# Performance work log

Hardware: AMD Instinct MI355X
Metric: run time of the kernel (lower is better)

Reference implementation:

```python
import jax, jax.numpy as jnp
import numpy as np

N_EMBD = 2048
N_HEAD = 16
HEAD_DIM = N_EMBD // N_HEAD
LORA_R = 8
LORA_ALPHA = 1.0
LORA_SCALING = LORA_ALPHA / LORA_R


def setup_inputs() -> dict:
    key = jax.random.key(0)
    ks = jax.random.split(key, 10)
    B, T = 4, 2048
    init = LORA_ALPHA / LORA_R
    return {
        "x": jax.random.normal(ks[0], (B, T, N_EMBD), dtype=jnp.float32),
        "W_attn": jax.random.normal(ks[1], (N_EMBD, 3 * N_EMBD), dtype=jnp.float32) * 0.02,
        "b_attn": jnp.zeros((3 * N_EMBD,), dtype=jnp.float32),
        "lora_A_q": jax.random.normal(ks[2], (N_EMBD, LORA_R), dtype=jnp.float32) * init,
        "lora_B_q": jax.random.normal(ks[3], (LORA_R, N_EMBD), dtype=jnp.float32) * init,
        "lora_A_k": jax.random.normal(ks[4], (N_EMBD, LORA_R), dtype=jnp.float32) * init,
        "lora_B_k": jax.random.normal(ks[5], (LORA_R, N_EMBD), dtype=jnp.float32) * init,
        "W_proj": jax.random.normal(ks[6], (N_EMBD, N_EMBD), dtype=jnp.float32) * 0.02,
        "b_proj": jnp.zeros((N_EMBD,), dtype=jnp.float32),
    }


def _rotate_half(x):
    # torch: x1 = x[..., ::2]; x2 = x[..., 1::2]; cat((-x2, x1), -1)
    x1 = x[..., ::2]
    x2 = x[..., 1::2]
    return jnp.concatenate([-x2, x1], axis=-1)


def _rope_cos_sin(T, dtype):
    inv_freq = 1.0 / (10000.0 ** (jnp.arange(0, HEAD_DIM, 2, dtype=jnp.float32) / HEAD_DIM))
    t = jnp.arange(T, dtype=jnp.float32)
    freqs = jnp.einsum("i,j->ij", t, inv_freq)            # [T, D/2]
    emb = jnp.concatenate([freqs, freqs], axis=-1)          # [T, D]
    return jnp.cos(emb).astype(dtype), jnp.sin(emb).astype(dtype)


def reference(x, W_attn, b_attn, lora_A_q, lora_B_q, lora_A_k, lora_B_k, W_proj, b_proj):
    B, T, C = x.shape
    qkv = x @ W_attn + b_attn                                # [B,T,3C]
    q, k, v = jnp.split(qkv, 3, axis=2)
    # LoRA additions on q, k (applied to attn outputs, per module)
    q = q + (q @ lora_A_q) @ lora_B_q * LORA_SCALING
    k = k + (k @ lora_A_k) @ lora_B_k * LORA_SCALING

    def to_heads(z):
        return z.reshape(B, T, N_HEAD, HEAD_DIM).transpose(0, 2, 1, 3)  # [B,H,T,D]

    q, k, v = to_heads(q), to_heads(k), to_heads(v)
    cos, sin = _rope_cos_sin(T, x.dtype)                     # [T,D] each
    q = q * cos + _rotate_half(q) * sin
    k = k * cos + _rotate_half(k) * sin

    scale = 1.0 / jnp.sqrt(jnp.asarray(HEAD_DIM, dtype=x.dtype))
    scores = jnp.einsum("bhqd,bhkd->bhqk", q, k) * scale     # [B,H,T,T]
    causal = jnp.tril(jnp.ones((T, T), dtype=bool))
    scores = jnp.where(causal, scores, jnp.finfo(x.dtype).min)
    attn = jax.nn.softmax(scores, axis=-1)
    y = jnp.einsum("bhqk,bhkd->bhqd", attn, v)               # [B,H,T,D]
    y = y.transpose(0, 2, 1, 3).reshape(B, T, C)
    return y @ W_proj + b_proj
```

## Files before the change

### kernel.cpp

```cpp
#include <hip/hip_runtime.h>
#include <stdint.h>


typedef __attribute__((ext_vector_type(8))) short short8;
typedef __attribute__((ext_vector_type(4))) short short4v;
typedef __attribute__((ext_vector_type(4))) float floatx4;

__device__ __forceinline__ float bf2f(short h) {
  union { unsigned int u; float f; } v;
  v.u = ((unsigned int)(unsigned short)h) << 16;
  return v.f;
}
__device__ __forceinline__ short f2bf(float f) {
  unsigned int u = __float_as_uint(f);
  unsigned int r = (u + 0x7FFFu + ((u >> 16) & 1u)) >> 16;
  return (short)r;
}

__device__ __forceinline__ void gload_lds16(const short* g, short* l) {
  __builtin_amdgcn_global_load_lds(
      (const __attribute__((address_space(1))) unsigned int*)g,
      (__attribute__((address_space(3))) unsigned int*)l, 16, 0, 0);
}

__device__ __forceinline__ void store_out(float* p, float v) { *p = v; }
__device__ __forceinline__ void store_out(short* p, float v) { *p = f2bf(v); }

__device__ __forceinline__ int xcd_swz(int orig, int nwg) {
  int q = nwg >> 3;
  return (orig & 7) * q + (orig >> 3);
}

#define SWZ(off, row) ((off) ^ (((row) & 7) << 3))

__global__ void k_f2b(const float* __restrict__ in, short* __restrict__ out, int n8) {
  int i = blockIdx.x * 256 + threadIdx.x;
  if (i >= n8) return;
  const float4* p = (const float4*)in + (size_t)i * 2;
  float4 a = p[0], b = p[1];
  short8 v;
  v[0] = f2bf(a.x); v[1] = f2bf(a.y); v[2] = f2bf(a.z); v[3] = f2bf(a.w);
  v[4] = f2bf(b.x); v[5] = f2bf(b.y); v[6] = f2bf(b.z); v[7] = f2bf(b.w);
  *(short8*)(out + (size_t)i * 8) = v;
}

__global__ void k_wT(const float* __restrict__ W, short* __restrict__ WT, int K, int N) {
  __shared__ float tile[32][33];
  int n0 = blockIdx.x * 32, k0 = blockIdx.y * 32;
  int tx = threadIdx.x, ty = threadIdx.y;
  #pragma unroll
  for (int i = 0; i < 4; i++)
    tile[ty + i * 8][tx] = W[(size_t)(k0 + ty + i * 8) * N + n0 + tx];
  __syncthreads();
  #pragma unroll
  for (int i = 0; i < 4; i++)
    WT[(size_t)(n0 + ty + i * 8) * K + k0 + tx] = f2bf(tile[tx][ty + i * 8]);
}

__global__ void k_ropetab(float* __restrict__ ct, float* __restrict__ st) {
  int t = blockIdx.x, j = threadIdx.x;
  float invf = powf(10000.0f, -(float)(2 * j) / 128.0f);
  float ang = (float)t * invf;
  ct[t * 64 + j] = cosf(ang);
  st[t * 64 + j] = sinf(ang);
}


#define GBAR __builtin_amdgcn_s_barrier();

#define RDA(QR) \
    _Pragma("unroll") for (int m_ = 0; m_ < 4; m_++) \
    _Pragma("unroll") for (int kk_ = 0; kk_ < 2; kk_++) { \
      int sA_ = ((QR) * 2 + wm) * 8192 + (m_ * 16 + c16) * 128 + kk_ * 64 + g * 16; \
      afr[m_][kk_] = *(const short8*)(Ab + ((sA_ ^ swzk) >> 1)); \
    }

#define RDB(QC, DST) \
    _Pragma("unroll") for (int n_ = 0; n_ < 2; n_++) \
    _Pragma("unroll") for (int kk_ = 0; kk_ < 2; kk_++) { \
      int sB_ = ((QC) * 4 + wn) * 4096 + (n_ * 16 + c16) * 128 + kk_ * 64 + g * 16; \
      DST[n_][kk_] = *(const short8*)(Bb + ((sB_ ^ swzk) >> 1)); \
    }

#define MM(QR, QC, BF) \
    __builtin_amdgcn_s_barrier(); \
    __builtin_amdgcn_s_setprio(1); \
    _Pragma("unroll") for (int kk_ = 0; kk_ < 2; kk_++) \
    _Pragma("unroll") for (int m_ = 0; m_ < 4; m_++) \
    _Pragma("unroll") for (int n_ = 0; n_ < 2; n_++) \
      acc[(QR) * 4 + m_][(QC) * 2 + n_] = __builtin_amdgcn_mfma_f32_16x16x32_bf16( \
          afr[m_][kk_], BF[n_][kk_], acc[(QR) * 4 + m_][(QC) * 2 + n_], 0, 0, 0); \
    __builtin_amdgcn_s_setprio(0);

template <typename OutT>
__global__ __launch_bounds__(512, 2) void k_gemm8(
    const short* __restrict__ A, const short* __restrict__ BT,
    const float* __restrict__ bias, OutT* __restrict__ C,
    int M, int N, int K)
{
  __shared__ __attribute__((aligned(16))) short lds[65536];
  const int tid = threadIdx.x;
  const int w = tid >> 6, l = tid & 63;
  const int g = l >> 4, c16 = l & 15;
  const int wm = w >> 2, wn = w & 3;
  const int swzk = (c16 & 7) << 4;

  const int nwg = gridDim.x * gridDim.y;
  const int wg = xcd_swz(blockIdx.y * gridDim.x + blockIdx.x, nwg);
  const int bm = wg % gridDim.x, bn = wg / gridDim.x;

  const short* Ablk = A + (size_t)bm * 256 * K;
  const short* Bblk = BT + (size_t)bn * 256 * K;

  floatx4 acc[8][4];
  #pragma unroll
  for (int i = 0; i < 8; i++)
    #pragma unroll
    for (int j = 0; j < 4; j++)
      acc[i][j] = (floatx4){0.f, 0.f, 0.f, 0.f};

  const int NT = K >> 6;
  const int L = NT >> 1;

  auto stageA = [&](int b, int h, int t) {
    short* dst = lds + b * 32768;
    int k0 = t * 64;
    #pragma unroll
    for (int j = 0; j < 2; j++) {
      int P = h * 2 + j;
      int sL = P * 8192 + tid * 16;
      int q = sL ^ (((sL >> 7) & 7) << 4);
      int row = (((((P & 1) << 1) | (P >> 1))) << 6) + ((sL >> 7) & 63);
      gload_lds16(Ablk + (size_t)row * K + k0 + ((q & 127) >> 1), dst + (sL >> 1));
    }
  };
  auto stageB = [&](int b, int h, int t) {
    short* dst = lds + b * 32768 + 16384;
    int k0 = t * 64;
    #pragma unroll
    for (int j = 0; j < 2; j++) {
      int sL = (h * 4 + 2 * j) * 4096 + tid * 16;
      int pos = sL >> 12;
      int q = sL ^ (((sL >> 7) & 7) << 4);
      int row = (((pos & 3) * 2 + (pos >> 2)) << 5) + ((sL >> 7) & 31);
      gload_lds16(Bblk + (size_t)row * K + k0 + ((q & 127) >> 1), dst + (sL >> 1));
    }
  };

  stageA(0, 0, 0); stageB(0, 0, 0); stageA(0, 1, 0); stageB(0, 1, 0);
  stageA(1, 0, 1); stageB(1, 0, 1); stageA(1, 1, 1); stageB(1, 1, 1);
  asm volatile("s_waitcnt vmcnt(8)" ::: "memory");
  __builtin_amdgcn_s_barrier();

  #pragma unroll 1
  for (int i = 0; i < L; i++) {
    const int t2 = 2 * i + 2, t3 = 2 * i + 3;
    short8 afr[4][2], bfr0[2][2], bfr1[2][2];

    {
      const short* Ab = lds;
      const short* Bb = lds + 16384;
      RDA(0) RDB(0, bfr0) if (i > 0) stageA(1, 1, 2 * i + 1);
      MM(0, 0, bfr0) GBAR
      RDB(1, bfr1) if (t2 < NT) stageA(0, 0, t2);
      MM(0, 1, bfr1) GBAR
      RDA(1) if (t2 < NT) stageB(0, 0, t2);
      MM(1, 0, bfr0) GBAR
      if (t2 < NT) stageB(0, 1, t2);
      MM(1, 1, bfr1)
      if (t2 < NT) { asm volatile("s_waitcnt vmcnt(6)" ::: "memory"); }
      else         { asm volatile("s_waitcnt vmcnt(0)" ::: "memory"); }
      GBAR
    }
    {
      const short* Ab = lds + 32768;
      const short* Bb = lds + 49152;
      RDA(0) RDB(0, bfr0) if (t2 < NT) stageA(0, 1, t2);
      MM(0, 0, bfr0) GBAR
      RDB(1, bfr1) if (t3 < NT) stageA(1, 0, t3);
      MM(0, 1, bfr1) GBAR
      RDA(1) if (t3 < NT) stageB(1, 0, t3);
      MM(1, 0, bfr0) GBAR
      if (t3 < NT) stageB(1, 1, t3);
      MM(1, 1, bfr1)
      if (t3 < NT) { asm volatile("s_waitcnt vmcnt(6)" ::: "memory"); }
      else         { asm volatile("s_waitcnt vmcnt(0)" ::: "memory"); }
      GBAR
    }
  }

  #pragma unroll
  for (int qr = 0; qr < 2; qr++)
    #pragma unroll
    for (int qc = 0; qc < 2; qc++)
      #pragma unroll
      for (int m = 0; m < 4; m++)
        #pragma unroll
        for (int n = 0; n < 2; n++) {
          int col = bn * 256 + wn * 64 + qc * 32 + n * 16 + c16;
          float bv = bias[col];
          #pragma unroll
          for (int r = 0; r < 4; r++) {
            size_t row = (size_t)bm * 256 + wm * 128 + qr * 64 + m * 16 + g * 4 + r;
            store_out(C + row * (size_t)N + col, acc[qr * 4 + m][qc * 2 + n][r] + bv);
          }
        }
}

__global__ __launch_bounds__(256, 2) void k_lorarope(
    short* __restrict__ qkv, const float* __restrict__ Aq, const float* __restrict__ Ak,
    const float* __restrict__ Bq, const float* __restrict__ Bk,
    const float* __restrict__ ct, const float* __restrict__ st)
{
  __shared__ float Bs[8 * 2048];
  __shared__ short Ls[2048];
  __shared__ float red[4][8];
  const int u = threadIdx.x;
  const int which = blockIdx.y;
  const float* Am = which ? Ak : Aq;
  const float* Bm = which ? Bk : Bq;
  const float qs = which ? 1.0f : 0.08838834764831845f;

  #pragma unroll
  for (int i = 0; i < 16; i++) {
    int idx = (i * 256 + u) * 4;
    *(float4*)(Bs + idx) = *(const float4*)(Bm + idx);
  }
  float Areg[8][8];
  #pragma unroll
  for (int e = 0; e < 8; e++) {
    float4 a0 = *(const float4*)(Am + (size_t)(u * 8 + e) * 8);
    float4 a1 = *(const float4*)(Am + (size_t)(u * 8 + e) * 8 + 4);
    Areg[e][0] = a0.x; Areg[e][1] = a0.y; Areg[e][2] = a0.z; Areg[e][3] = a0.w;
    Areg[e][4] = a1.x; Areg[e][5] = a1.y; Areg[e][6] = a1.z; Areg[e][7] = a1.w;
  }
  __syncthreads();

  const int wv = u >> 6, l = u & 63;
  const int h = u >> 4, j0 = (u & 15) * 4;
  const int base = h * 128;
  const int t0 = blockIdx.x * 32;

  for (int tt = 0; tt < 32; tt++) {
    const int tok = t0 + tt;
    const int trow = tok & 2047;
    short* row = qkv + (size_t)tok * 6144 + which * 2048;

    __syncthreads();

    short8 q8 = *(const short8*)(row + u * 8);
    *(short8*)(Ls + u * 8) = q8;
    float part[8];
    #pragma unroll
    for (int r = 0; r < 8; r++) part[r] = 0.f;
    #pragma unroll
    for (int e = 0; e < 8; e++) {
      float qv = bf2f(q8[e]);
      #pragma unroll
      for (int r = 0; r < 8; r++) part[r] += qv * Areg[e][r];
    }
    #pragma unroll
    for (int r = 0; r < 8; r++)
      for (int off = 32; off > 0; off >>= 1)
        part[r] += __shfl_xor(part[r], off);
    if (l == 0) {
      #pragma unroll
      for (int r = 0; r < 8; r++) red[wv][r] = part[r];
    }
    __syncthreads();

    float Tr[8];
    #pragma unroll
    for (int r = 0; r < 8; r++)
      Tr[r] = (red[0][r] + red[1][r] + red[2][r] + red[3][r]) * 0.125f;

    float4 cv = *(const float4*)(ct + trow * 64 + j0);
    float4 sv = *(const float4*)(st + trow * 64 + j0);
    short4v qa4 = *(const short4v*)(Ls + base + j0);
    short4v qb4 = *(const short4v*)(Ls + base + 64 + j0);
    short8 qeo = *(const short8*)(Ls + base + 2 * j0);

    float o1[4], o2[4];
    #pragma unroll
    for (int j = 0; j < 4; j++) {
      float da = 0.f, db = 0.f, de = 0.f, dd = 0.f;
      #pragma unroll
      for (int r = 0; r < 8; r++) {
        const float* Br = Bs + r * 2048 + base;
        da += Tr[r] * Br[j0 + j];
        db += Tr[r] * Br[64 + j0 + j];
        de += Tr[r] * Br[2 * (j0 + j)];
        dd += Tr[r] * Br[2 * (j0 + j) + 1];
      }
      float qa = bf2f(qa4[j]) + da;
      float qb = bf2f(qb4[j]) + db;
      float qe = bf2f(qeo[2 * j]) + de;
      float qo = bf2f(qeo[2 * j + 1]) + dd;
      float c = ((const float*)&cv)[j], s = ((const float*)&sv)[j];
      o1[j] = (qa * c - qo * s) * qs;
      o2[j] = (qb * c + qe * s) * qs;
    }
    short4v w1, w2;
    #pragma unroll
    for (int j = 0; j < 4; j++) { w1[j] = f2bf(o1[j]); w2[j] = f2bf(o2[j]); }
    *(short4v*)(row + base + j0) = w1;
    *(short4v*)(row + base + 64 + j0) = w2;
  }
}

__global__ void k_vt(const short* __restrict__ qkv, short* __restrict__ vT) {
  __shared__ short tile[32][33];
  int bh = blockIdx.z, b = bh >> 4, h = bh & 15;
  int t0 = blockIdx.x * 32, d0 = blockIdx.y * 32;
  int tx = threadIdx.x, ty = threadIdx.y;
  #pragma unroll
  for (int i = 0; i < 4; i++) {
    int tt = t0 + ty + i * 8;
    tile[ty + i * 8][tx] = qkv[(size_t)(b * 2048 + tt) * 6144 + 4096 + h * 128 + d0 + tx];
  }
  __syncthreads();
  #pragma unroll
  for (int i = 0; i < 4; i++) {
    int d = d0 + ty + i * 8;
    vT[((size_t)bh * 128 + d) * 2048 + t0 + tx] = tile[tx][ty + i * 8];
  }
}

__global__ __launch_bounds__(256, 2) void k_attn(
    const short* __restrict__ qkv, const short* __restrict__ vT, short* __restrict__ y)
{
  __shared__ __attribute__((aligned(16))) short Ks[64 * 128];
  __shared__ __attribute__((aligned(16))) short Vs[128 * 64];
  __shared__ __attribute__((aligned(16))) short Ps[4 * 32 * 64];
  const int bh = blockIdx.x, b = bh >> 4, h = bh & 15;
  const int qt = 15 - (int)blockIdx.y;
  const int t = threadIdx.x, w = t >> 6, l = t & 63, g = l >> 4, c16 = l & 15;

  const int skr = t >> 2, sc0 = (t & 3) * 32;
  const int svd = t >> 1, sv0 = (t & 1) * 32;
  const short* kbase = qkv + (size_t)(b * 2048) * 6144 + 2048 + h * 128;
  const short* vbase = vT + (size_t)bh * 128 * 2048;
  short* Pw = Ps + w * (32 * 64);

  short8 onesv;
  #pragma unroll
  for (int e = 0; e < 8; e++) onesv[e] = (short)0x3F80;

  short8 qf[2][4];
  #pragma unroll
  for (int m = 0; m < 2; m++) {
    size_t goff = (size_t)(b * 2048 + qt * 128 + w * 32 + m * 16 + c16) * 6144 + h * 128;
    #pragma unroll
    for (int kf = 0; kf < 4; kf++)
      qf[m][kf] = *(const short8*)(qkv + goff + kf * 32 + 8 * g);
  }

  floatx4 o[2][8], ls[2];
  float mrow[2][4];
  #pragma unroll
  for (int m = 0; m < 2; m++) {
    #pragma unroll
    for (int nf = 0; nf < 8; nf++) o[m][nf] = (floatx4){0.f, 0.f, 0.f, 0.f};
    ls[m] = (floatx4){0.f, 0.f, 0.f, 0.f};
    #pragma unroll
    for (int r = 0; r < 4; r++) mrow[m][r] = -1e30f;
  }

  const int ntiles = 2 * qt + 2;

  short8 kreg[4], vreg[4];
  #pragma unroll
  for (int ii = 0; ii < 4; ii++) {
    kreg[ii] = *(const short8*)(kbase + (size_t)skr * 6144 + sc0 + ii * 8);
    vreg[ii] = *(const short8*)(vbase + (size_t)svd * 2048 + sv0 + ii * 8);
  }

  for (int kt = 0; kt < ntiles; kt++) {
    __syncthreads();
    #pragma unroll
    for (int ii = 0; ii < 4; ii++) {
      *(short8*)(Ks + SWZ(skr * 128 + sc0 + ii * 8, skr)) = kreg[ii];
      *(short8*)(Vs + SWZ(svd * 64 + sv0 + ii * 8, svd)) = vreg[ii];
    }
    __syncthreads();

    if (kt + 1 < ntiles) {
      #pragma unroll
      for (int ii = 0; ii < 4; ii++) {
        kreg[ii] = *(const short8*)(kbase + (size_t)((kt + 1) * 64 + skr) * 6144 + sc0 + ii * 8);
        vreg[ii] = *(const short8*)(vbase + (size_t)svd * 2048 + (kt + 1) * 64 + sv0 + ii * 8);
      }
    }

    floatx4 sc[2][4];
    #pragma unroll
    for (int m = 0; m < 2; m++)
      #pragma unroll
      for (int nf = 0; nf < 4; nf++) sc[m][nf] = (floatx4){0.f, 0.f, 0.f, 0.f};
    __builtin_amdgcn_s_setprio(1);
    #pragma unroll
    for (int kf = 0; kf < 4; kf++)
      #pragma unroll
      for (int nf = 0; nf < 4; nf++) {
        short8 kb = *(const short8*)(Ks + SWZ((nf * 16 + c16) * 128 + kf * 32 + 8 * g, c16));
        sc[0][nf] = __builtin_amdgcn_mfma_f32_16x16x32_bf16(qf[0][kf], kb, sc[0][nf], 0, 0, 0);
        sc[1][nf] = __builtin_amdgcn_mfma_f32_16x16x32_bf16(qf[1][kf], kb, sc[1][nf], 0, 0, 0);
      }
    __builtin_amdgcn_s_setprio(0);

    if (kt >= 2 * qt) {
      #pragma unroll
      for (int m = 0; m < 2; m++)
        #pragma unroll
        for (int nf = 0; nf < 4; nf++) {
          int key = kt * 64 + nf * 16 + c16;
          #pragma unroll
          for (int r = 0; r < 4; r++) {
            int qr = qt * 128 + w * 32 + m * 16 + g * 4 + r;
            if (key > qr) sc[m][nf][r] = -1e30f;
          }
        }
    }

    float rmv[2][4];
    float need = -1e30f;
    #pragma unroll
    for (int m = 0; m < 2; m++)
      #pragma unroll
      for (int r = 0; r < 4; r++) {
        float rm = fmaxf(fmaxf(sc[m][0][r], sc[m][1][r]), fmaxf(sc[m][2][r], sc[m][3][r]));
        rm = fmaxf(rm, __shfl_xor(rm, 1));
        rm = fmaxf(rm, __shfl_xor(rm, 2));
        rm = fmaxf(rm, __shfl_xor(rm, 4));
        rm = fmaxf(rm, __shfl_xor(rm, 8));
        rmv[m][r] = rm;
        need = fmaxf(need, rm - mrow[m][r]);
      }
    if (!__all(need <= 8.0f)) {
      #pragma unroll
      for (int m = 0; m < 2; m++) {
        #pragma unroll
        for (int r = 0; r < 4; r++) {
          float mn = fmaxf(mrow[m][r], rmv[m][r]);
          float al = __expf(mrow[m][r] - mn);
          mrow[m][r] = mn;
          ls[m][r] *= al;
          #pragma unroll
          for (int nf = 0; nf < 8; nf++) o[m][nf][r] *= al;
        }
      }
    }
    #pragma unroll
    for (int m = 0; m < 2; m++)
      #pragma unroll
      for (int r = 0; r < 4; r++) {
        int prow = m * 16 + g * 4 + r;
        #pragma unroll
        for (int nf = 0; nf < 4; nf++) {
          float p = __expf(sc[m][nf][r] - mrow[m][r]);
          Pw[SWZ(prow * 64 + nf * 16 + c16, prow)] = f2bf(p);
        }
      }

    short8 pa[2][2];
    #pragma unroll
    for (int m = 0; m < 2; m++)
      #pragma unroll
      for (int kf = 0; kf < 2; kf++)
        pa[m][kf] = *(const short8*)(Pw + SWZ((m * 16 + c16) * 64 + kf * 32 + 8 * g, c16));
    __builtin_amdgcn_s_setprio(1);
    #pragma unroll
    for (int m = 0; m < 2; m++)
      #pragma unroll
      for (int kf = 0; kf < 2; kf++)
        ls[m] = __builtin_amdgcn_mfma_f32_16x16x32_bf16(pa[m][kf], onesv, ls[m], 0, 0, 0);
    #pragma unroll
    for (int kf = 0; kf < 2; kf++)
      #pragma unroll
      for (int nf = 0; nf < 8; nf++) {
        short8 vb = *(const short8*)(Vs + SWZ((nf * 16 + c16) * 64 + kf * 32 + 8 * g, c16));
        o[0][nf] = __builtin_amdgcn_mfma_f32_16x16x32_bf16(pa[0][kf], vb, o[0][nf], 0, 0, 0);
        o[1][nf] = __builtin_amdgcn_mfma_f32_16x16x32_bf16(pa[1][kf], vb, o[1][nf], 0, 0, 0);
      }
    __builtin_amdgcn_s_setprio(0);
  }

  #pragma unroll
  for (int m = 0; m < 2; m++) {
    float ri[4];
    #pragma unroll
    for (int r = 0; r < 4; r++) ri[r] = 1.0f / ls[m][r];
    size_t yr0 = (size_t)(b * 2048 + qt * 128 + w * 32 + m * 16 + g * 4);
    #pragma unroll
    for (int nf = 0; nf < 8; nf++) {
      int col = h * 128 + nf * 16 + c16;
      #pragma unroll
      for (int r = 0; r < 4; r++)
        y[(yr0 + r) * 2048 + col] = f2bf(o[m][nf][r] * ri[r]);
    }
  }
}

extern "C" void kernel_launch(void* const* d_in, const int* in_sizes, int n_in,
                              void* d_out, int out_size, void* d_ws, size_t ws_size,
                              hipStream_t stream) {
  (void)in_sizes; (void)n_in; (void)out_size; (void)ws_size;
  const float* x      = (const float*)d_in[0];
  const float* W_attn = (const float*)d_in[1];
  const float* b_attn = (const float*)d_in[2];
  const float* Aq     = (const float*)d_in[3];
  const float* Bq     = (const float*)d_in[4];
  const float* Ak     = (const float*)d_in[5];
  const float* Bk     = (const float*)d_in[6];
  const float* W_proj = (const float*)d_in[7];
  const float* b_proj = (const float*)d_in[8];

  char* ws = (char*)d_ws;
  short* xb  = (short*)(ws + 0);
  short* WTa = (short*)(ws + 33554432);
  short* WTp = (short*)(ws + 58720256);
  short* qkv = (short*)(ws + 67108864);
  float* ct  = (float*)(ws + 168296448);
  float* st  = (float*)(ws + 168820736);
  short* vT  = (short*)(ws + 169345024);
  short* y   = xb;

  k_f2b<<<8192, 256, 0, stream>>>(x, xb, 2097152);
  k_wT<<<dim3(192, 64), dim3(32, 8), 0, stream>>>(W_attn, WTa, 2048, 6144);
  k_wT<<<dim3(64, 64), dim3(32, 8), 0, stream>>>(W_proj, WTp, 2048, 2048);
  k_ropetab<<<2048, 64, 0, stream>>>(ct, st);
  k_gemm8<short><<<dim3(32, 24), 512, 0, stream>>>(xb, WTa, b_attn, qkv, 8192, 6144, 2048);
  k_lorarope<<<dim3(256, 2), 256, 0, stream>>>(qkv, Aq, Ak, Bq, Bk, ct, st);
  k_vt<<<dim3(64, 4, 64), dim3(32, 8), 0, stream>>>(qkv, vT);
  k_attn<<<dim3(64, 16), 256, 0, stream>>>(qkv, vT, y);
  k_gemm8<float><<<dim3(32, 8), 512, 0, stream>>>(y, WTp, b_proj, (float*)d_out, 8192, 2048, 2048);
}
```

Measured before the change: 612.4 us.

## Prefetch GEMM B fragments across phases, use exp2 softmax with log2e-folded scale

The GEMM main loop now reads the first B fragment of the next half-tile before the last MFMA block, and reorders the waits and stage issues to match, so LDS reads overlap MFMA work. The attention kernel folds log2(e) into the query scale so it can call the hardware exp2 instead of __expf. It raises the lazy-rescale threshold to match the base-2 units and swaps the hand-rolled bf16 rounding for the library conversion. The prefetch reorder changes the vmcnt accounting and barrier placement, which risks ordering mistakes.

Result: no change. 604.1 us (-1.3%).

```diff
diff --git a/kernel.cpp b/kernel.cpp
--- a/kernel.cpp
+++ b/kernel.cpp
@@ -1,10 +1,13 @@
 #include <hip/hip_runtime.h>
+#include <hip/hip_bf16.h>
 #include <stdint.h>
 
 
 typedef __attribute__((ext_vector_type(8))) short short8;
 typedef __attribute__((ext_vector_type(4))) short short4v;
 typedef __attribute__((ext_vector_type(4))) float floatx4;
+
+#define EXP2F(x) __builtin_amdgcn_exp2f(x)
 
 __device__ __forceinline__ float bf2f(short h) {
   union { unsigned int u; float f; } v;
@@ -15,6 +18,10 @@
   unsigned int u = __float_as_uint(f);
   unsigned int r = (u + 0x7FFFu + ((u >> 16) & 1u)) >> 16;
   return (short)r;
+}
+__device__ __forceinline__ short f2bf_n(float f) {
+  __hip_bfloat16 h = __float2bfloat16(f);
+  union { __hip_bfloat16 b; short s; } v; v.b = h; return v.s;
 }
 
 __device__ __forceinline__ void gload_lds16(const short* g, short* l) {
@@ -75,11 +82,11 @@
       afr[m_][kk_] = *(const short8*)(Ab + ((sA_ ^ swzk) >> 1)); \
     }
 
-#define RDB(QC, DST) \
+#define RDBX(BB, QC, DST) \
     _Pragma("unroll") for (int n_ = 0; n_ < 2; n_++) \
     _Pragma("unroll") for (int kk_ = 0; kk_ < 2; kk_++) { \
       int sB_ = ((QC) * 4 + wn) * 4096 + (n_ * 16 + c16) * 128 + kk_ * 64 + g * 16; \
-      DST[n_][kk_] = *(const short8*)(Bb + ((sB_ ^ swzk) >> 1)); \
+      DST[n_][kk_] = *(const short8*)((BB) + ((sB_ ^ swzk) >> 1)); \
     }
 
 #define MM(QR, QC, BF) \
@@ -152,40 +159,42 @@
   asm volatile("s_waitcnt vmcnt(8)" ::: "memory");
   __builtin_amdgcn_s_barrier();
 
+  short8 bfr0[2][2], bfr1[2][2];
+  RDBX(lds + 16384, 0, bfr0)
+
   #pragma unroll 1
   for (int i = 0; i < L; i++) {
     const int t2 = 2 * i + 2, t3 = 2 * i + 3;
-    short8 afr[4][2], bfr0[2][2], bfr1[2][2];
+    short8 afr[4][2];
 
     {
       const short* Ab = lds;
-      const short* Bb = lds + 16384;
-      RDA(0) RDB(0, bfr0) if (i > 0) stageA(1, 1, 2 * i + 1);
+      RDA(0) if (i > 0) stageA(1, 1, 2 * i + 1);
       MM(0, 0, bfr0) GBAR
-      RDB(1, bfr1) if (t2 < NT) stageA(0, 0, t2);
+      RDBX(lds + 16384, 1, bfr1) if (t2 < NT) stageA(0, 0, t2);
       MM(0, 1, bfr1) GBAR
       RDA(1) if (t2 < NT) stageB(0, 0, t2);
-      MM(1, 0, bfr0) GBAR
-      if (t2 < NT) stageB(0, 1, t2);
-      MM(1, 1, bfr1)
-      if (t2 < NT) { asm volatile("s_waitcnt vmcnt(6)" ::: "memory"); }
+      MM(1, 0, bfr0)
+      if (t2 < NT) { asm volatile("s_waitcnt vmcnt(4)" ::: "memory"); }
       else         { asm volatile("s_waitcnt vmcnt(0)" ::: "memory"); }
       GBAR
+      RDBX(lds + 49152, 0, bfr0) if (t2 < NT) stageB(0, 1, t2);
+      MM(1, 1, bfr1) GBAR
     }
     {
       const short* Ab = lds + 32768;
-      const short* Bb = lds + 49152;
-      RDA(0) RDB(0, bfr0) if (t2 < NT) stageA(0, 1, t2);
+      RDA(0) if (t2 < NT) stageA(0, 1, t2);
       MM(0, 0, bfr0) GBAR
-      RDB(1, bfr1) if (t3 < NT) stageA(1, 0, t3);
+      RDBX(lds + 49152, 1, bfr1) if (t3 < NT) stageA(1, 0, t3);
       MM(0, 1, bfr1) GBAR
       RDA(1) if (t3 < NT) stageB(1, 0, t3);
-      MM(1, 0, bfr0) GBAR
-      if (t3 < NT) stageB(1, 1, t3);
-      MM(1, 1, bfr1)
-      if (t3 < NT) { asm volatile("s_waitcnt vmcnt(6)" ::: "memory"); }
+      MM(1, 0, bfr0)
+      if (t3 < NT) { asm volatile("s_waitcnt vmcnt(4)" ::: "memory"); }
       else         { asm volatile("s_waitcnt vmcnt(0)" ::: "memory"); }
       GBAR
+      if (t2 < NT) { RDBX(lds + 16384, 0, bfr0) }
+      if (t3 < NT) stageB(1, 1, t3);
+      MM(1, 1, bfr1) GBAR
     }
   }
 
@@ -219,7 +228,7 @@
   const int which = blockIdx.y;
   const float* Am = which ? Ak : Aq;
   const float* Bm = which ? Bk : Bq;
-  const float qs = which ? 1.0f : 0.08838834764831845f;
+  const float qs = which ? 1.0f : 0.127517403f;
 
   #pragma unroll
   for (int i = 0; i < 16; i++) {
@@ -436,13 +445,13 @@
         rmv[m][r] = rm;
         need = fmaxf(need, rm - mrow[m][r]);
       }
-    if (!__all(need <= 8.0f)) {
+    if (!__all(need <= 11.0f)) {
       #pragma unroll
       for (int m = 0; m < 2; m++) {
         #pragma unroll
         for (int r = 0; r < 4; r++) {
           float mn = fmaxf(mrow[m][r], rmv[m][r]);
-          float al = __expf(mrow[m][r] - mn);
+          float al = EXP2F(mrow[m][r] - mn);
           mrow[m][r] = mn;
           ls[m][r] *= al;
           #pragma unroll
@@ -457,8 +466,8 @@
         int prow = m * 16 + g * 4 + r;
         #pragma unroll
         for (int nf = 0; nf < 4; nf++) {
-          float p = __expf(sc[m][nf][r] - mrow[m][r]);
-          Pw[SWZ(prow * 64 + nf * 16 + c16, prow)] = f2bf(p);
+          float p = EXP2F(sc[m][nf][r] - mrow[m][r]);
+          Pw[SWZ(prow * 64 + nf * 16 + c16, prow)] = f2bf_n(p);
         }
       }
 
@@ -496,7 +505,7 @@
       int col = h * 128 + nf * 16 + c16;
       #pragma unroll
       for (int r = 0; r < 4; r++)
-        y[(yr0 + r) * 2048 + col] = f2bf(o[m][nf][r] * ri[r]);
+        y[(yr0 + r) * 2048 + col] = f2bf_n(o[m][nf][r] * ri[r]);
     }
   }
 }
```
